# Kernel optimization log

Measured on AMD Instinct MI355X. Metric: run time of the kernel, lower is better.

Reference implementation:

```python
import jax, jax.numpy as jnp
import numpy as np

BN_EPS = 1e-5
CUT_THRESH = 1e-3  # cut_conv1 zeroes a channel plane if its abs-max < 0.001


def setup_inputs() -> dict:
    key = jax.random.key(0)
    k1, k2, k3 = jax.random.split(key, 3)
    B, Cin, Cout, H, W, K = 32, 32, 32, 192, 192, 3
    return {
        "x": jax.random.normal(k1, (B, Cin, H, W), dtype=jnp.float32),
        "conv_w": jax.random.normal(k2, (Cout, Cin, K, K), dtype=jnp.float32) * 0.05,
        "conv_b": jax.random.normal(k3, (Cout,), dtype=jnp.float32) * 0.05,
        "gamma": jnp.ones((Cout,), dtype=jnp.float32),
        "beta": jnp.zeros((Cout,), dtype=jnp.float32),
        "run_mean": jnp.zeros((Cout,), dtype=jnp.float32),
        "run_var": jnp.ones((Cout,), dtype=jnp.float32),
    }


def reference(x, conv_w, conv_b, gamma, beta, run_mean, run_var):
    # Conv2d, stride 1, padding 1 (NCHW / OIHW)
    y = jax.lax.conv_general_dilated(
        x, conv_w, window_strides=(1, 1), padding=((1, 1), (1, 1)),
        dimension_numbers=("NCHW", "OIHW", "NCHW"))
    y = y + conv_b[None, :, None, None]
    # BatchNorm2d (inference form with running stats)
    inv_std = gamma * jax.lax.rsqrt(run_var + BN_EPS)
    y = (y - run_mean[None, :, None, None]) * inv_std[None, :, None, None] \
        + beta[None, :, None, None]
    # ReLU
    y = jnp.maximum(y, 0.0)
    # cut_conv1: per (batch, channel) abs-max; zero whole plane if below threshold.
    # Vectorized replacement of the original B*C Python loop.
    chan_absmax = jnp.max(jnp.abs(y), axis=(2, 3), keepdims=True)  # [B, C, 1, 1]
    return jnp.where(chan_absmax < CUT_THRESH, jnp.zeros_like(y), y)
```

## Files before the change

### kernel.cpp

```cpp
#include <hip/hip_runtime.h>

typedef short short8 __attribute__((ext_vector_type(8)));
typedef float f32x4 __attribute__((ext_vector_type(4)));

#define BN_EPS 1e-5f
#define CUT_THRESH 1e-3f

#define WS_COEF 18432
#define WS_PART 18688

__device__ __forceinline__ unsigned short f2bf(float f) {
  unsigned u = __float_as_uint(f);
  u += 0x7FFFu + ((u >> 16) & 1u);
  return (unsigned short)(u >> 16);
}

__device__ __forceinline__ void gload_lds16(const void* g, void* l) {
  __builtin_amdgcn_global_load_lds(
      (const __attribute__((address_space(1))) unsigned int*)g,
      (__attribute__((address_space(3))) unsigned int*)l, 16, 0, 0);
}

__global__ void prep_kernel(const float* __restrict__ wgt,
                            const float* __restrict__ bias,
                            const float* __restrict__ gamma,
                            const float* __restrict__ beta,
                            const float* __restrict__ rmean,
                            const float* __restrict__ rvar,
                            unsigned short* __restrict__ wbf,
                            float* __restrict__ coef) {
  int tid = blockIdx.x * 256 + threadIdx.x;
  if (tid < 9216) {
    int co = tid / 288;
    int rem = tid - co * 288;
    int ci = rem / 9;
    int kk = rem - ci * 9;
    int oct = ((ci >> 3) ^ ((co >> 1) & 3)) << 3;
    wbf[(kk * 32 + co) * 32 + oct + (ci & 7)] = f2bf(wgt[tid]);
  }
  if (tid < 32) {
    float s = gamma[tid] * rsqrtf(rvar[tid] + BN_EPS);
    coef[tid] = s;
    coef[32 + tid] = (bias[tid] - rmean[tid]) * s + beta[tid];
  }
}

template <bool INTERIOR>
__device__ __forceinline__ void stage_x(const float* __restrict__ xb, int r0,
                                        int c0, int tid, int m80,
                                        unsigned short* __restrict__ lx) {
  float fv[6][8];
  int lofs[6];
  int okm[6];
#pragma unroll
  for (int r = 0; r < 6; ++r) {
    int id = (r < 5) ? (r * 256 + tid) : (1280 + m80);
    int g = id & 3;
    int p = id >> 2;
    int h = p / 34;
    int w = p - h * 34;
    const float* src;
    if (INTERIOR) {
      okm[r] = -1;
      src = xb + (g * 8) * 36864 + (r0 - 1 + h) * 192 + (c0 - 1 + w);
    } else {
      int gh = r0 - 1 + h, gw = c0 - 1 + w;
      okm[r] = (((unsigned)gh < 192u) && ((unsigned)gw < 192u)) ? -1 : 0;
      int ghc = min(max(gh, 0), 191);
      int gwc = min(max(gw, 0), 191);
      src = xb + (g * 8) * 36864 + ghc * 192 + gwc;
    }
#pragma unroll
    for (int j = 0; j < 8; ++j) fv[r][j] = src[j * 36864];
    lofs[r] = p * 32 + ((g ^ ((w >> 1) & 3)) << 3);
  }
  __builtin_amdgcn_sched_barrier(0);

#pragma unroll
  for (int r = 0; r < 6; ++r) {
    unsigned pk[4];
#pragma unroll
    for (int q = 0; q < 4; ++q) {
      float f0 = fv[r][2 * q], f1 = fv[r][2 * q + 1];
      if (!INTERIOR) {
        f0 = okm[r] ? f0 : 0.f;
        f1 = okm[r] ? f1 : 0.f;
      }
      unsigned a = __float_as_uint(f0) + 0x8000u;
      unsigned c = __float_as_uint(f1) + 0x8000u;
      pk[q] = __builtin_amdgcn_perm(c, a, 0x07060302u);
    }
    short8 v;
    reinterpret_cast<unsigned*>(&v)[0] = pk[0];
    reinterpret_cast<unsigned*>(&v)[1] = pk[1];
    reinterpret_cast<unsigned*>(&v)[2] = pk[2];
    reinterpret_cast<unsigned*>(&v)[3] = pk[3];
    *reinterpret_cast<short8*>(&lx[lofs[r]]) = v;
  }
}

__global__ __launch_bounds__(256, 3) void conv_bn_relu_kernel(
    const float* __restrict__ x,
    const unsigned short* __restrict__ wbf,
    const float* __restrict__ coef,
    float* __restrict__ out,
    float* __restrict__ part) {
  __shared__ unsigned short lx[10 * 34 * 32];
  __shared__ unsigned short lw[9 * 32 * 32];

  int bid = blockIdx.x;
  int orig = (bid & 7) * 576 + (bid >> 3);
  int b = orig / 144;
  int t = orig - b * 144;
  int tr = t / 6, tc = t - tr * 6;
  int r0 = tr * 8, c0 = tc * 32;
  int tid = threadIdx.x;

  {
    const short8* wsrc = reinterpret_cast<const short8*>(wbf);
    short8* wdst = reinterpret_cast<short8*>(lw);
#pragma unroll
    for (int r = 0; r < 4; ++r) gload_lds16(wsrc + r * 256 + tid, wdst + r * 256 + tid);
    if (tid < 128) gload_lds16(wsrc + 1024 + tid, wdst + 1024 + tid);
  }

  const float* xb = x + b * (32 * 192 * 192);
  int m80 = tid;
  m80 = (m80 >= 160) ? m80 - 160 : m80;
  m80 = (m80 >= 80) ? m80 - 80 : m80;

  if (tr >= 1 && tr <= 22 && tc >= 1 && tc <= 4)
    stage_x<true>(xb, r0, c0, tid, m80, lx);
  else
    stage_x<false>(xb, r0, c0, tid, m80, lx);

  int lane = tid & 63;
  int wv = tid >> 6;
  int l15 = lane & 15;
  int lg = lane >> 4;

  f32x4 scl[2], sft[2];
#pragma unroll
  for (int m = 0; m < 2; ++m) {
    scl[m] = *reinterpret_cast<const f32x4*>(coef + m * 16 + lg * 4);
    sft[m] = *reinterpret_cast<const f32x4*>(coef + 32 + m * 16 + lg * 4);
  }

  __syncthreads();

  int aswz = (lg ^ ((l15 >> 1) & 3)) << 3;
  f32x4 acc[2][4] = {};

#pragma unroll
  for (int s = 0; s < 9; ++s) {
    const int kh = s / 3, kw = s - kh * 3;
    short8 A0 = *reinterpret_cast<const short8*>(&lw[(s * 32 + l15) * 32 + aswz]);
    short8 A1 = *reinterpret_cast<const short8*>(&lw[(s * 32 + 16 + l15) * 32 + aswz]);
#pragma unroll
    for (int n = 0; n < 4; ++n) {
      int hl = 2 * wv + (n >> 1) + kh;
      int wl = ((n & 1) << 4) + l15 + kw;
      short8 Bf = *reinterpret_cast<const short8*>(
          &lx[(hl * 34 + wl) * 32 + ((lg ^ ((wl >> 1) & 3)) << 3)]);
      acc[0][n] = __builtin_amdgcn_mfma_f32_16x16x32_bf16(A0, Bf, acc[0][n], 0, 0, 0);
      acc[1][n] = __builtin_amdgcn_mfma_f32_16x16x32_bf16(A1, Bf, acc[1][n], 0, 0, 0);
    }
  }

  const int HW = 192 * 192;
  float* ob = out + b * 32 * HW;
  float pmax[2][4];
#pragma unroll
  for (int m = 0; m < 2; ++m)
#pragma unroll
    for (int j = 0; j < 4; ++j) pmax[m][j] = 0.f;

#pragma unroll
  for (int m = 0; m < 2; ++m)
#pragma unroll
    for (int n = 0; n < 4; ++n) {
      int gr = r0 + 2 * wv + (n >> 1);
      int gc = c0 + ((n & 1) << 4) + l15;
#pragma unroll
      for (int j = 0; j < 4; ++j) {
        int co = m * 16 + lg * 4 + j;
        float v = fmaxf(acc[m][n][j] * scl[m][j] + sft[m][j], 0.f);
        __builtin_nontemporal_store(v, &ob[co * HW + gr * 192 + gc]);
        pmax[m][j] = fmaxf(pmax[m][j], v);
      }
    }

#pragma unroll
  for (int m = 0; m < 2; ++m)
#pragma unroll
    for (int j = 0; j < 4; ++j) {
      float v = pmax[m][j];
      v = fmaxf(v, __shfl_xor(v, 1, 16));
      v = fmaxf(v, __shfl_xor(v, 2, 16));
      v = fmaxf(v, __shfl_xor(v, 4, 16));
      v = fmaxf(v, __shfl_xor(v, 8, 16));
      if (l15 == 0) {
        int co = m * 16 + lg * 4 + j;
        __builtin_nontemporal_store(v, &part[((size_t)b * 32 + co) * 576 + t * 4 + wv]);
      }
    }
}

__global__ __launch_bounds__(256) void cut_kernel(float* __restrict__ out,
                                                  const float* __restrict__ part) {
  __shared__ float r4[4];
  int p = blockIdx.x;
  const float* pp = part + (size_t)p * 576;
  float m = 0.f;
  for (int i = threadIdx.x; i < 576; i += 256) m = fmaxf(m, pp[i]);
#pragma unroll
  for (int k = 1; k < 64; k <<= 1) m = fmaxf(m, __shfl_xor(m, k, 64));
  if ((threadIdx.x & 63) == 0) r4[threadIdx.x >> 6] = m;
  __syncthreads();
  m = fmaxf(fmaxf(r4[0], r4[1]), fmaxf(r4[2], r4[3]));
  if (m >= CUT_THRESH) return;
  float* base = out + (size_t)p * 36864;
  for (int i = threadIdx.x; i < 36864; i += 256) base[i] = 0.f;
}

extern "C" void kernel_launch(void* const* d_in, const int* in_sizes, int n_in,
                              void* d_out, int out_size, void* d_ws, size_t ws_size,
                              hipStream_t stream) {
  const float* x     = (const float*)d_in[0];
  const float* wgt   = (const float*)d_in[1];
  const float* bias  = (const float*)d_in[2];
  const float* gamma = (const float*)d_in[3];
  const float* beta  = (const float*)d_in[4];
  const float* rmean = (const float*)d_in[5];
  const float* rvar  = (const float*)d_in[6];
  float* out = (float*)d_out;

  unsigned short* wbf  = (unsigned short*)d_ws;
  float*          coef = (float*)((char*)d_ws + WS_COEF);
  float*          part = (float*)((char*)d_ws + WS_PART);

  prep_kernel<<<36, 256, 0, stream>>>(wgt, bias, gamma, beta, rmean, rvar, wbf, coef);
  conv_bn_relu_kernel<<<4608, 256, 0, stream>>>(x, wbf, coef, out, part);
  cut_kernel<<<1024, 256, 0, stream>>>(out, part);
}
```

Before: 77.98 us.

## Switch conv MFMA from 16x16x32 to 32x32x16 tiles and raise occupancy hint

Replaces the 16x16x32 bf16 MFMA tiling (2 co-blocks by 4 pixel blocks) with 32x32x16 MFMAs covering all 32 output channels by 32 columns per row, two rows per wave. The A and B fragment loads, the epilogue channel mapping and the partial abs-max layout change to match. The partial buffer doubles to 1152 entries per plane and the cut kernel reads it accordingly. Launch bounds go from 3 to 4 blocks per CU. The aim is fewer MFMA issues and LDS reads per output, traded against a different store pattern and added register pressure.

New measurement: 73.95 us. 1.05x faster.

```diff
diff --git a/kernel.cpp b/kernel.cpp
--- a/kernel.cpp
+++ b/kernel.cpp
@@ -2,6 +2,7 @@
 
 typedef short short8 __attribute__((ext_vector_type(8)));
 typedef float f32x4 __attribute__((ext_vector_type(4)));
+typedef float f32x16 __attribute__((ext_vector_type(16)));
 
 #define BN_EPS 1e-5f
 #define CUT_THRESH 1e-3f
@@ -99,7 +100,7 @@
   }
 }
 
-__global__ __launch_bounds__(256, 3) void conv_bn_relu_kernel(
+__global__ __launch_bounds__(256, 4) void conv_bn_relu_kernel(
     const float* __restrict__ x,
     const unsigned short* __restrict__ wbf,
     const float* __restrict__ coef,
@@ -136,83 +137,88 @@
 
   int lane = tid & 63;
   int wv = tid >> 6;
-  int l15 = lane & 15;
-  int lg = lane >> 4;
-
-  f32x4 scl[2], sft[2];
-#pragma unroll
-  for (int m = 0; m < 2; ++m) {
-    scl[m] = *reinterpret_cast<const f32x4*>(coef + m * 16 + lg * 4);
-    sft[m] = *reinterpret_cast<const f32x4*>(coef + 32 + m * 16 + lg * 4);
+  int w_ = lane & 31;
+  int lh = lane >> 5;
+  int coA = lane & 31;
+
+  f32x4 scl4[4], sft4[4];
+#pragma unroll
+  for (int g = 0; g < 4; ++g) {
+    scl4[g] = *reinterpret_cast<const f32x4*>(coef + g * 8 + 4 * lh);
+    sft4[g] = *reinterpret_cast<const f32x4*>(coef + 32 + g * 8 + 4 * lh);
   }
 
   __syncthreads();
 
-  int aswz = (lg ^ ((l15 >> 1) & 3)) << 3;
-  f32x4 acc[2][4] = {};
+  const int akey = (coA >> 1) & 3;
+  f32x16 acc[2] = {};
 
 #pragma unroll
   for (int s = 0; s < 9; ++s) {
     const int kh = s / 3, kw = s - kh * 3;
-    short8 A0 = *reinterpret_cast<const short8*>(&lw[(s * 32 + l15) * 32 + aswz]);
-    short8 A1 = *reinterpret_cast<const short8*>(&lw[(s * 32 + 16 + l15) * 32 + aswz]);
-#pragma unroll
-    for (int n = 0; n < 4; ++n) {
-      int hl = 2 * wv + (n >> 1) + kh;
-      int wl = ((n & 1) << 4) + l15 + kw;
-      short8 Bf = *reinterpret_cast<const short8*>(
-          &lx[(hl * 34 + wl) * 32 + ((lg ^ ((wl >> 1) & 3)) << 3)]);
-      acc[0][n] = __builtin_amdgcn_mfma_f32_16x16x32_bf16(A0, Bf, acc[0][n], 0, 0, 0);
-      acc[1][n] = __builtin_amdgcn_mfma_f32_16x16x32_bf16(A1, Bf, acc[1][n], 0, 0, 0);
+    short8 A0 = *reinterpret_cast<const short8*>(
+        &lw[(s * 32 + coA) * 32 + ((lh ^ akey) << 3)]);
+    short8 A1 = *reinterpret_cast<const short8*>(
+        &lw[(s * 32 + coA) * 32 + (((2 + lh) ^ akey) << 3)]);
+    int wl = w_ + kw;
+    int bkey = (wl >> 1) & 3;
+#pragma unroll
+    for (int rr = 0; rr < 2; ++rr) {
+      int hl = 2 * wv + rr + kh;
+      const unsigned short* brow = &lx[(hl * 34 + wl) * 32];
+      short8 B0 = *reinterpret_cast<const short8*>(brow + ((lh ^ bkey) << 3));
+      short8 B1 = *reinterpret_cast<const short8*>(brow + (((2 + lh) ^ bkey) << 3));
+      acc[rr] = __builtin_amdgcn_mfma_f32_32x32x16_bf16(A0, B0, acc[rr], 0, 0, 0);
+      acc[rr] = __builtin_amdgcn_mfma_f32_32x32x16_bf16(A1, B1, acc[rr], 0, 0, 0);
     }
   }
 
   const int HW = 192 * 192;
   float* ob = out + b * 32 * HW;
-  float pmax[2][4];
-#pragma unroll
-  for (int m = 0; m < 2; ++m)
-#pragma unroll
-    for (int j = 0; j < 4; ++j) pmax[m][j] = 0.f;
-
-#pragma unroll
-  for (int m = 0; m < 2; ++m)
-#pragma unroll
-    for (int n = 0; n < 4; ++n) {
-      int gr = r0 + 2 * wv + (n >> 1);
-      int gc = c0 + ((n & 1) << 4) + l15;
-#pragma unroll
-      for (int j = 0; j < 4; ++j) {
-        int co = m * 16 + lg * 4 + j;
-        float v = fmaxf(acc[m][n][j] * scl[m][j] + sft[m][j], 0.f);
-        __builtin_nontemporal_store(v, &ob[co * HW + gr * 192 + gc]);
-        pmax[m][j] = fmaxf(pmax[m][j], v);
-      }
-    }
-
-#pragma unroll
-  for (int m = 0; m < 2; ++m)
-#pragma unroll
-    for (int j = 0; j < 4; ++j) {
-      float v = pmax[m][j];
-      v = fmaxf(v, __shfl_xor(v, 1, 16));
-      v = fmaxf(v, __shfl_xor(v, 2, 16));
-      v = fmaxf(v, __shfl_xor(v, 4, 16));
-      v = fmaxf(v, __shfl_xor(v, 8, 16));
-      if (l15 == 0) {
-        int co = m * 16 + lg * 4 + j;
-        __builtin_nontemporal_store(v, &part[((size_t)b * 32 + co) * 576 + t * 4 + wv]);
-      }
-    }
+  float pmax[16];
+#pragma unroll
+  for (int r = 0; r < 16; ++r) pmax[r] = 0.f;
+
+#pragma unroll
+  for (int rr = 0; rr < 2; ++rr) {
+    int gr = r0 + 2 * wv + rr;
+    float* rowp = ob + gr * 192 + c0 + w_;
+#pragma unroll
+    for (int r = 0; r < 16; ++r) {
+      int co = (r & 3) + 8 * (r >> 2) + 4 * lh;
+      float v = fmaxf(acc[rr][r] * scl4[r >> 2][r & 3] + sft4[r >> 2][r & 3], 0.f);
+      __builtin_nontemporal_store(v, rowp + co * HW);
+      pmax[r] = fmaxf(pmax[r], v);
+    }
+  }
+
+#pragma unroll
+  for (int r = 0; r < 16; ++r) {
+    float v = pmax[r];
+    v = fmaxf(v, __shfl_xor(v, 1, 32));
+    v = fmaxf(v, __shfl_xor(v, 2, 32));
+    v = fmaxf(v, __shfl_xor(v, 4, 32));
+    v = fmaxf(v, __shfl_xor(v, 8, 32));
+    pmax[r] = v;
+  }
+  if ((lane & 15) == 0) {
+    int subl = (lane >> 4) & 1;
+#pragma unroll
+    for (int r = 0; r < 16; ++r) {
+      int co = (r & 3) + 8 * (r >> 2) + 4 * lh;
+      __builtin_nontemporal_store(
+          pmax[r], &part[((size_t)b * 32 + co) * 1152 + t * 8 + wv * 2 + subl]);
+    }
+  }
 }
 
 __global__ __launch_bounds__(256) void cut_kernel(float* __restrict__ out,
                                                   const float* __restrict__ part) {
   __shared__ float r4[4];
   int p = blockIdx.x;
-  const float* pp = part + (size_t)p * 576;
+  const float* pp = part + (size_t)p * 1152;
   float m = 0.f;
-  for (int i = threadIdx.x; i < 576; i += 256) m = fmaxf(m, pp[i]);
+  for (int i = threadIdx.x; i < 1152; i += 256) m = fmaxf(m, pp[i]);
 #pragma unroll
   for (int k = 1; k < 64; k <<= 1) m = fmaxf(m, __shfl_xor(m, k, 64));
   if ((threadIdx.x & 63) == 0) r4[threadIdx.x >> 6] = m;
```
